# Performance work log

Measured on AMD Instinct MI355X. Metric: run time of the kernel, lower is better.

Reference implementation:

```python
import jax, jax.numpy as jnp
import numpy as np

N_HEADS = 12

def setup_inputs() -> dict:
    key = jax.random.key(0)
    ks = jax.random.split(key, 3)
    B, C, T = 4, 768, 2048
    x = jax.random.normal(ks[0], (B, C, T), dtype=jnp.float32)
    mask = jnp.ones((B, 1, 1, T), dtype=jnp.int32)  # all valid; masked_fill where mask==0
    Wqkv = jax.random.normal(ks[1], (3 * C, C), dtype=jnp.float32) * 0.02
    bqkv = jnp.zeros((3 * C,), dtype=jnp.float32)
    Wout = jax.random.normal(ks[2], (C, C), dtype=jnp.float32) * 0.02
    bout = jnp.zeros((C,), dtype=jnp.float32)
    return {"x": x, "mask": mask, "Wqkv": Wqkv, "bqkv": bqkv, "Wout": Wout, "bout": bout}


def reference(x, mask, Wqkv, bqkv, Wout, bout):
    B, C, T = x.shape
    H = N_HEADS
    d = C // H
    scale = 1.0 / jnp.sqrt(jnp.asarray(d, x.dtype))
    # 1x1 Conv1d == per-timestep matmul over channels
    qkv = jnp.einsum('oc,bct->bot', Wqkv, x) + bqkv[None, :, None]  # [B,3C,T]
    # channel dim splits as [3, H, d] per the torch view(B,3,H,d,T)
    qkv = qkv.reshape(B, 3, H, d, T).transpose(0, 1, 2, 4, 3)       # [B,3,H,T,d]
    q, k, v = qkv[:, 0], qkv[:, 1], qkv[:, 2]
    score = jnp.einsum('bhtd,bhsd->bhts', q, k) * scale             # [B,H,T,T]
    score = jnp.where(mask == 0, jnp.asarray(-10000.0, score.dtype), score)
    attn = jax.nn.softmax(score, axis=-1)  # dropout: eval mode (identity)
    o = jnp.einsum('bhts,bhsd->bhtd', attn, v)                      # [B,H,T,d]
    o = o.transpose(0, 1, 3, 2).reshape(B, C, T)                    # [B,C,T]
    return jnp.einsum('oc,bct->bot', Wout, o) + bout[None, :, None]
```

## Files before the change

kernel.cpp:

```cpp
#include <hip/hip_runtime.h>
#include <hip/hip_bf16.h>
#include <stdint.h>

#define B_   4
#define C_   768
#define T_   2048
#define H_   12
#define D_   64
#define O3_  2304

typedef __attribute__((ext_vector_type(4))) float f32x4;
typedef __attribute__((ext_vector_type(8))) short bf16x8;

__device__ __forceinline__ unsigned short f2bf(float f) {
  union { float f; unsigned int u; } v; v.f = f;
  unsigned int r = v.u + 0x7fffu + ((v.u >> 16) & 1u);
  return (unsigned short)(r >> 16);
}

__device__ __forceinline__ unsigned int pack2bf(float a, float b) {
  __hip_bfloat162 h2 = __float22bfloat162_rn(make_float2(a, b));
  union { __hip_bfloat162 h; unsigned int u; } cv; cv.h = h2;
  return cv.u;
}

__device__ __forceinline__ float fexp2(float x) {
#if __has_builtin(__builtin_amdgcn_exp2f)
  return __builtin_amdgcn_exp2f(x);
#else
  return exp2f(x);
#endif
}

__device__ __forceinline__ void async16(const void* g, void* lds) {
#if __has_builtin(__builtin_amdgcn_global_load_lds)
  __builtin_amdgcn_global_load_lds((const __attribute__((address_space(1))) void*)g,
                                   (__attribute__((address_space(3))) void*)lds, 16, 0, 0);
#else
  int lane = threadIdx.x & 63;
  *((uint4*)((char*)lds + lane * 16)) = *((const uint4*)g);
#endif
}


__global__ void cvt_f32_bf16(const float* __restrict__ in,
                             unsigned short* __restrict__ out, int n4) {
  int i = blockIdx.x * 256 + threadIdx.x;
  if (i < n4) {
    float4 f = ((const float4*)in)[i];
    ushort4 o;
    o.x = f2bf(f.x); o.y = f2bf(f.y); o.z = f2bf(f.z); o.w = f2bf(f.w);
    ((ushort4*)out)[i] = o;
  }
}

__global__ void make_bias(const int* __restrict__ mask, float* __restrict__ mbias, int n) {
  int i = blockIdx.x * 256 + threadIdx.x;
  if (i < n) mbias[i] = (mask[i] == 0) ? -14426.950408f : 0.0f;
}

__global__ void transpose_x(const float* __restrict__ x,
                            unsigned short* __restrict__ xT) {
  __shared__ unsigned short tile[32][33];
  int b = blockIdx.z;
  int c0 = blockIdx.y * 32;
  int t0 = blockIdx.x * 32;
  int tid = threadIdx.x;
  {
    int cl = tid >> 3;
    int tl = (tid & 7) * 4;
    float4 f = *(const float4*)(x + ((size_t)b * C_ + c0 + cl) * T_ + t0 + tl);
    tile[tl + 0][cl] = f2bf(f.x);
    tile[tl + 1][cl] = f2bf(f.y);
    tile[tl + 2][cl] = f2bf(f.z);
    tile[tl + 3][cl] = f2bf(f.w);
  }
  __syncthreads();
  {
    int tl = tid >> 3;
    int cl = (tid & 7) * 4;
    ushort4 o;
    o.x = tile[tl][cl + 0]; o.y = tile[tl][cl + 1];
    o.z = tile[tl][cl + 2]; o.w = tile[tl][cl + 3];
    *(ushort4*)(xT + ((size_t)b * T_ + t0 + tl) * C_ + c0 + cl) = o;
  }
}

__global__ __launch_bounds__(256)
void gemm_qkv(const unsigned short* __restrict__ xT,
              const unsigned short* __restrict__ W1,
              const float* __restrict__ bqkv,
              unsigned short* __restrict__ Qb,
              unsigned short* __restrict__ Kb,
              unsigned short* __restrict__ Vb) {
  __shared__ unsigned short sA[2][128 * 32];
  __shared__ unsigned short sB[2][128 * 32];

  const int b   = blockIdx.z;
  const int o0  = blockIdx.y * 128;
  const int t0  = blockIdx.x * 128;
  const int tid = threadIdx.x;
  const int wave = tid >> 6, lane = tid & 63;
  const int q = lane >> 4, ln = lane & 15;
  const int tw = wave >> 1, ow = wave & 1;

  const unsigned short* Ax = xT + (size_t)b * T_ * C_;
  const int srow = lane >> 2;
  const int scol = (lane & 3) * 8;

  const f32x4 ZERO = {0.f, 0.f, 0.f, 0.f};
  f32x4 acc[4][4];
#pragma unroll
  for (int mi = 0; mi < 4; ++mi)
#pragma unroll
    for (int ni = 0; ni < 4; ++ni) acc[mi][ni] = ZERO;

#pragma unroll
  for (int j = 0; j < 2; ++j) {
    const int chunk = wave * 2 + j;
    const int row = chunk * 16 + srow;
    async16(Ax + (size_t)(t0 + row) * C_ + scol, &sA[0][chunk * 512]);
    async16(W1 + (size_t)(o0 + row) * C_ + scol, &sB[0][chunk * 512]);
  }

  for (int i = 0; i < 24; ++i) {
    const int buf = i & 1;
    __syncthreads();
    if (i < 23) {
      const int k0 = (i + 1) * 32;
#pragma unroll
      for (int j = 0; j < 2; ++j) {
        const int chunk = wave * 2 + j;
        const int row = chunk * 16 + srow;
        async16(Ax + (size_t)(t0 + row) * C_ + k0 + scol, &sA[buf ^ 1][chunk * 512]);
        async16(W1 + (size_t)(o0 + row) * C_ + k0 + scol, &sB[buf ^ 1][chunk * 512]);
      }
    }

    bf16x8 aF[4], bF[4];
#pragma unroll
    for (int mi = 0; mi < 4; ++mi)
      aF[mi] = *(const bf16x8*)(&sA[buf][(tw * 64 + mi * 16 + ln) * 32 + q * 8]);
#pragma unroll
    for (int ni = 0; ni < 4; ++ni)
      bF[ni] = *(const bf16x8*)(&sB[buf][(ow * 64 + ni * 16 + ln) * 32 + q * 8]);
#pragma unroll
    for (int mi = 0; mi < 4; ++mi)
#pragma unroll
      for (int ni = 0; ni < 4; ++ni)
        acc[mi][ni] = __builtin_amdgcn_mfma_f32_16x16x32_bf16(aF[mi], bF[ni], acc[mi][ni], 0, 0, 0);
  }

  const float QSCL = 0.125f * 1.44269504f;
#pragma unroll
  for (int ni = 0; ni < 4; ++ni) {
    const int o = o0 + ow * 64 + ni * 16 + ln;
    const float bias = bqkv[o];
    const int which = o / C_;
    const int rem = o - which * C_;
    const int bh = b * H_ + (rem >> 6);
    const int dd = rem & 63;
#pragma unroll
    for (int mi = 0; mi < 4; ++mi) {
      const int tb = t0 + tw * 64 + mi * 16 + q * 4;
      f32x4 v = acc[mi][ni];
      if (which == 0) {
#pragma unroll
        for (int r = 0; r < 4; ++r)
          Qb[((size_t)bh * T_ + tb + r) * D_ + dd] = f2bf((v[r] + bias) * QSCL);
      } else if (which == 1) {
#pragma unroll
        for (int r = 0; r < 4; ++r) {
          const int s = tb + r;
          const int cp = (dd >> 3) ^ (s & 7);
          Kb[((size_t)bh * T_ + s) * 64 + (cp << 3) + (dd & 7)] = f2bf(v[r] + bias);
        }
      } else {
        const int tile = tb >> 6, si = tb & 63;
        const int cp = (si >> 3) ^ (dd & 7);
        ushort4 pk;
        pk.x = f2bf(v[0] + bias);
        pk.y = f2bf(v[1] + bias);
        pk.z = f2bf(v[2] + bias);
        pk.w = f2bf(v[3] + bias);
        *(ushort4*)(Vb + (((size_t)bh * 32 + tile) * 64 + dd) * 64 + (cp << 3) + (si & 7)) = pk;
      }
    }
  }
}

__global__ __launch_bounds__(256, 3)
void attn(const unsigned short* __restrict__ Qb,
          const unsigned short* __restrict__ Kb,
          const unsigned short* __restrict__ Vb,
          const float* __restrict__ mbias,
          unsigned short* __restrict__ Ob) {
  __shared__ __align__(16) char smem[53248];
  unsigned short* sK0 = (unsigned short*)smem;
  unsigned short* sV0 = (unsigned short*)(smem + 16384);

  const int id = blockIdx.x;
  const int bh = id % 48;
  const int tblk = id / 48;
  const int b = bh / H_, h = bh % H_;
  const int tid = threadIdx.x, wave = tid >> 6, lane = tid & 63;
  const int q = lane >> 4, ln = lane & 15;
  const int wj = wave & 1, si = wave >> 1;
  const int t0w = tblk * 128 + wj * 64;
  unsigned short* sPw = (unsigned short*)(smem + 32768 + wave * 5120);

  bf16x8 Qa[4][2];
#pragma unroll
  for (int tt = 0; tt < 4; ++tt) {
    const unsigned short* qrow = Qb + ((size_t)bh * T_ + t0w + tt * 16 + ln) * D_;
    Qa[tt][0] = *(const bf16x8*)(qrow + q * 8);
    Qa[tt][1] = *(const bf16x8*)(qrow + 32 + q * 8);
  }

  const f32x4 ZERO = {0.f, 0.f, 0.f, 0.f};
  f32x4 Oacc[4][4];
  f32x4 lacc[4];
#pragma unroll
  for (int dt = 0; dt < 4; ++dt)
#pragma unroll
    for (int tt = 0; tt < 4; ++tt) Oacc[dt][tt] = ZERO;
#pragma unroll
  for (int tt = 0; tt < 4; ++tt) lacc[tt] = ZERO;

  const short one_s = (ln == 0) ? (short)0x3F80 : (short)0;
  bf16x8 ones;
#pragma unroll
  for (int j = 0; j < 8; ++j) ones[j] = one_s;

  const unsigned short* gK = Kb + (size_t)bh * T_ * 64;
  const unsigned short* gV = Vb + (size_t)bh * 32 * 4096;

#pragma unroll
  for (int j = 0; j < 2; ++j) {
    const int chunk = wave * 2 + j;
    async16(gK + chunk * 512 + lane * 8, sK0 + chunk * 512);
    async16(gV + chunk * 512 + lane * 8, sV0 + chunk * 512);
  }

  for (int it = 0; it < 32; ++it) {
    const int buf = it & 1;
    __syncthreads();
    if (it < 31) {
      const unsigned short* k = gK + (it + 1) * 4096;
      const unsigned short* v = gV + (it + 1) * 4096;
      unsigned short* dK = sK0 + (buf ^ 1) * 4096;
      unsigned short* dV = sV0 + (buf ^ 1) * 4096;
#pragma unroll
      for (int j = 0; j < 2; ++j) {
        const int chunk = wave * 2 + j;
        async16(k + chunk * 512 + lane * 8, dK + chunk * 512);
        async16(v + chunk * 512 + lane * 8, dV + chunk * 512);
      }
    }

    const int s0 = it * 64;
    const float bvl = mbias[b * T_ + s0 + lane];
    const bool anymask = (__ballot(bvl != 0.0f) != 0ull);
    const unsigned short* sKc = sK0 + buf * 4096;
    const unsigned short* sVc = sV0 + buf * 4096;

#pragma unroll
    for (int sb = 0; sb < 2; ++sb) {
      const unsigned short* krow = sKc + (si * 32 + sb * 16 + ln) * 64;
      bf16x8 kf0 = *(const bf16x8*)(krow + ((q ^ (ln & 7)) << 3));
      bf16x8 kf1 = *(const bf16x8*)(krow + (((4 + q) ^ (ln & 7)) << 3));
      f32x4 bb = ZERO;
      if (anymask) bb = *(const f32x4*)(mbias + b * T_ + s0 + si * 32 + sb * 16 + q * 4);
#pragma unroll
      for (int tt = 0; tt < 4; ++tt) {
        f32x4 p0 = __builtin_amdgcn_mfma_f32_16x16x32_bf16(kf0, Qa[tt][0], ZERO, 0, 0, 0);
        f32x4 sc = __builtin_amdgcn_mfma_f32_16x16x32_bf16(kf1, Qa[tt][1], p0, 0, 0, 0);
        if (anymask) {
#pragma unroll
          for (int r = 0; r < 4; ++r) sc[r] += bb[r];
        }
        uint2 w;
        w.x = pack2bf(fexp2(sc[0]), fexp2(sc[1]));
        w.y = pack2bf(fexp2(sc[2]), fexp2(sc[3]));
        *(uint2*)(sPw + (tt * 16 + ln) * 40 + sb * 16 + q * 4) = w;
      }
    }

    bf16x8 vf[4];
#pragma unroll
    for (int dt = 0; dt < 4; ++dt)
      vf[dt] = *(const bf16x8*)(sVc + (dt * 16 + ln) * 64 +
                                (((si * 4 + q) ^ (ln & 7)) << 3));
#pragma unroll
    for (int tt = 0; tt < 4; ++tt) {
      bf16x8 pf = *(const bf16x8*)(sPw + (tt * 16 + ln) * 40 + q * 8);
      lacc[tt] = __builtin_amdgcn_mfma_f32_16x16x32_bf16(ones, pf, lacc[tt], 0, 0, 0);
#pragma unroll
      for (int dt = 0; dt < 4; ++dt)
        Oacc[dt][tt] = __builtin_amdgcn_mfma_f32_16x16x32_bf16(vf[dt], pf, Oacc[dt][tt], 0, 0, 0);
    }
  }

  __syncthreads();
  float* fbuf = (float*)smem;
  float* lbuf = (float*)(smem + 34816);
  if (si == 1) {
#pragma unroll
    for (int tt = 0; tt < 4; ++tt) {
#pragma unroll
      for (int dt = 0; dt < 4; ++dt)
        *(f32x4*)(fbuf + ((size_t)(wj * 64 + tt * 16 + ln)) * 68 + dt * 16 + q * 4) = Oacc[dt][tt];
      if (q == 0) lbuf[wj * 64 + tt * 16 + ln] = lacc[tt][0];
    }
  }
  __syncthreads();
  if (si == 0) {
#pragma unroll
    for (int tt = 0; tt < 4; ++tt) {
      const float lv = __shfl(lacc[tt][0], ln, 64) + lbuf[wj * 64 + tt * 16 + ln];
      const float inv = 1.0f / lv;
      const int t = t0w + tt * 16 + ln;
#pragma unroll
      for (int dt = 0; dt < 4; ++dt) {
        f32x4 o = Oacc[dt][tt];
        f32x4 p = *(const f32x4*)(fbuf + ((size_t)(wj * 64 + tt * 16 + ln)) * 68 + dt * 16 + q * 4);
        ushort4 pk;
        pk.x = f2bf((o[0] + p[0]) * inv);
        pk.y = f2bf((o[1] + p[1]) * inv);
        pk.z = f2bf((o[2] + p[2]) * inv);
        pk.w = f2bf((o[3] + p[3]) * inv);
        *(ushort4*)(Ob + ((size_t)b * T_ + t) * C_ + h * D_ + dt * 16 + q * 4) = pk;
      }
    }
  }
}

__global__ __launch_bounds__(256)
void gemm_out(const unsigned short* __restrict__ Ob,
              const unsigned short* __restrict__ W2,
              const float* __restrict__ bout,
              float* __restrict__ out) {
  __shared__ unsigned short sA[2][128 * 32];
  __shared__ unsigned short sB[2][128 * 32];

  const int b   = blockIdx.z;
  const int o0  = blockIdx.y * 128;
  const int t0  = blockIdx.x * 128;
  const int tid = threadIdx.x;
  const int wave = tid >> 6, lane = tid & 63;
  const int q = lane >> 4, ln = lane & 15;
  const int tw = wave >> 1, ow = wave & 1;

  const unsigned short* Bo = Ob + (size_t)b * T_ * C_;
  const int srow = lane >> 2;
  const int scol = (lane & 3) * 8;

  const f32x4 ZERO = {0.f, 0.f, 0.f, 0.f};
  f32x4 acc[4][4];
#pragma unroll
  for (int mi = 0; mi < 4; ++mi)
#pragma unroll
    for (int ni = 0; ni < 4; ++ni) acc[mi][ni] = ZERO;

#pragma unroll
  for (int j = 0; j < 2; ++j) {
    const int chunk = wave * 2 + j;
    const int row = chunk * 16 + srow;
    async16(W2 + (size_t)(o0 + row) * C_ + scol, &sA[0][chunk * 512]);
    async16(Bo + (size_t)(t0 + row) * C_ + scol, &sB[0][chunk * 512]);
  }

  for (int i = 0; i < 24; ++i) {
    const int buf = i & 1;
    __syncthreads();
    if (i < 23) {
      const int k0 = (i + 1) * 32;
#pragma unroll
      for (int j = 0; j < 2; ++j) {
        const int chunk = wave * 2 + j;
        const int row = chunk * 16 + srow;
        async16(W2 + (size_t)(o0 + row) * C_ + k0 + scol, &sA[buf ^ 1][chunk * 512]);
        async16(Bo + (size_t)(t0 + row) * C_ + k0 + scol, &sB[buf ^ 1][chunk * 512]);
      }
    }

    bf16x8 aF[4], bF[4];
#pragma unroll
    for (int mi = 0; mi < 4; ++mi)
      aF[mi] = *(const bf16x8*)(&sA[buf][(tw * 64 + mi * 16 + ln) * 32 + q * 8]);
#pragma unroll
    for (int ni = 0; ni < 4; ++ni)
      bF[ni] = *(const bf16x8*)(&sB[buf][(ow * 64 + ni * 16 + ln) * 32 + q * 8]);
#pragma unroll
    for (int mi = 0; mi < 4; ++mi)
#pragma unroll
      for (int ni = 0; ni < 4; ++ni)
        acc[mi][ni] = __builtin_amdgcn_mfma_f32_16x16x32_bf16(aF[mi], bF[ni], acc[mi][ni], 0, 0, 0);
  }

#pragma unroll
  for (int mi = 0; mi < 4; ++mi) {
    const int ob = o0 + tw * 64 + mi * 16 + q * 4;
#pragma unroll
    for (int ni = 0; ni < 4; ++ni) {
      const int t = t0 + ow * 64 + ni * 16 + ln;
      f32x4 v = acc[mi][ni];
#pragma unroll
      for (int r = 0; r < 4; ++r)
        out[((size_t)b * C_ + ob + r) * T_ + t] = v[r] + bout[ob + r];
    }
  }
}


extern "C" void kernel_launch(void* const* d_in, const int* in_sizes, int n_in,
                              void* d_out, int out_size, void* d_ws, size_t ws_size,
                              hipStream_t stream) {
  (void)in_sizes; (void)n_in; (void)out_size; (void)ws_size;
  const float* x    = (const float*)d_in[0];
  const int*   mask = (const int*)d_in[1];
  const float* Wqkv = (const float*)d_in[2];
  const float* bqkv = (const float*)d_in[3];
  const float* Wout = (const float*)d_in[4];
  const float* bout = (const float*)d_in[5];
  float* out = (float*)d_out;

  const size_t szHead = (size_t)B_ * H_ * T_ * D_;
  const size_t szBTC  = (size_t)B_ * T_ * C_;
  unsigned short* Qb  = (unsigned short*)d_ws;
  unsigned short* Kb  = Qb + szHead;
  unsigned short* Vb  = Kb + szHead;
  unsigned short* Ob  = Vb + szHead;
  unsigned short* xT  = Ob + szBTC;
  unsigned short* W1b = xT + szBTC;
  unsigned short* W2b = W1b + (size_t)O3_ * C_;
  float* mbias        = (float*)(W2b + (size_t)C_ * C_);

  cvt_f32_bf16<<<dim3((O3_ * C_ / 4 + 255) / 256), 256, 0, stream>>>(Wqkv, W1b, O3_ * C_ / 4);
  cvt_f32_bf16<<<dim3((C_ * C_ / 4 + 255) / 256), 256, 0, stream>>>(Wout, W2b, C_ * C_ / 4);
  make_bias<<<dim3((B_ * T_ + 255) / 256), 256, 0, stream>>>(mask, mbias, B_ * T_);
  transpose_x<<<dim3(T_ / 32, C_ / 32, B_), 256, 0, stream>>>(x, xT);
  gemm_qkv<<<dim3(T_ / 128, O3_ / 128, B_), 256, 0, stream>>>(xT, W1b, bqkv, Qb, Kb, Vb);
  attn<<<dim3(768), 256, 0, stream>>>(Qb, Kb, Vb, mbias, Ob);
  gemm_out<<<dim3(T_ / 128, C_ / 128, B_), 256, 0, stream>>>(Ob, W2b, bout, out);
}
```

Baseline: 238.0 us.

## Keep softmax probabilities in registers via fp16 MFMA and split keys across four waves

The attention kernel now gives each block 64 queries and splits every 64-key tile across four waves of 16 keys each. Exponentiated scores are packed into fp16 registers and fed straight to 16x16x16 f16 MFMAs, with V stored in fp16, so the LDS round-trip for P and the ones-vector MFMA for the row sum are gone. The row sum is accumulated in scalar registers and reduced with shuffles. The grid doubles, LDS drops so more blocks fit per CU, and the partial outputs of the four waves are reduced through fp16 LDS buffers, which costs extra cross-wave reduction and precision.

New measurement: 327.5 us. 37.6% more time.

```diff
diff --git a/kernel.cpp b/kernel.cpp
--- a/kernel.cpp
+++ b/kernel.cpp
@@ -11,6 +11,8 @@
 
 typedef __attribute__((ext_vector_type(4))) float f32x4;
 typedef __attribute__((ext_vector_type(8))) short bf16x8;
+typedef __attribute__((ext_vector_type(4))) _Float16 f16x4;
+typedef __attribute__((ext_vector_type(2))) __fp16 h16x2;
 
 __device__ __forceinline__ unsigned short f2bf(float f) {
   union { float f; unsigned int u; } v; v.f = f;
@@ -18,10 +20,12 @@
   return (unsigned short)(r >> 16);
 }
 
-__device__ __forceinline__ unsigned int pack2bf(float a, float b) {
-  __hip_bfloat162 h2 = __float22bfloat162_rn(make_float2(a, b));
-  union { __hip_bfloat162 h; unsigned int u; } cv; cv.h = h2;
-  return cv.u;
+__device__ __forceinline__ unsigned short f2h(float f) {
+  union { _Float16 h; unsigned short u; } c; c.h = (_Float16)f; return c.u;
+}
+
+__device__ __forceinline__ float h2f(unsigned short u) {
+  union { _Float16 h; unsigned short u; } c; c.u = u; return (float)c.h;
 }
 
 __device__ __forceinline__ float fexp2(float x) {
@@ -179,23 +183,23 @@
         const int tile = tb >> 6, si = tb & 63;
         const int cp = (si >> 3) ^ (dd & 7);
         ushort4 pk;
-        pk.x = f2bf(v[0] + bias);
-        pk.y = f2bf(v[1] + bias);
-        pk.z = f2bf(v[2] + bias);
-        pk.w = f2bf(v[3] + bias);
+        pk.x = f2h(v[0] + bias);
+        pk.y = f2h(v[1] + bias);
+        pk.z = f2h(v[2] + bias);
+        pk.w = f2h(v[3] + bias);
         *(ushort4*)(Vb + (((size_t)bh * 32 + tile) * 64 + dd) * 64 + (cp << 3) + (si & 7)) = pk;
       }
     }
   }
 }
 
-__global__ __launch_bounds__(256, 3)
+__global__ __launch_bounds__(256, 4)
 void attn(const unsigned short* __restrict__ Qb,
           const unsigned short* __restrict__ Kb,
           const unsigned short* __restrict__ Vb,
           const float* __restrict__ mbias,
           unsigned short* __restrict__ Ob) {
-  __shared__ __align__(16) char smem[53248];
+  __shared__ __align__(16) char smem[32768];
   unsigned short* sK0 = (unsigned short*)smem;
   unsigned short* sV0 = (unsigned short*)(smem + 16384);
 
@@ -203,41 +207,32 @@
   const int bh = id % 48;
   const int tblk = id / 48;
   const int b = bh / H_, h = bh % H_;
-  const int tid = threadIdx.x, wave = tid >> 6, lane = tid & 63;
+  const int tid = threadIdx.x, si = tid >> 6, lane = tid & 63;
   const int q = lane >> 4, ln = lane & 15;
-  const int wj = wave & 1, si = wave >> 1;
-  const int t0w = tblk * 128 + wj * 64;
-  unsigned short* sPw = (unsigned short*)(smem + 32768 + wave * 5120);
+  const int t0 = tblk * 64;
 
   bf16x8 Qa[4][2];
 #pragma unroll
   for (int tt = 0; tt < 4; ++tt) {
-    const unsigned short* qrow = Qb + ((size_t)bh * T_ + t0w + tt * 16 + ln) * D_;
+    const unsigned short* qrow = Qb + ((size_t)bh * T_ + t0 + tt * 16 + ln) * D_;
     Qa[tt][0] = *(const bf16x8*)(qrow + q * 8);
     Qa[tt][1] = *(const bf16x8*)(qrow + 32 + q * 8);
   }
 
   const f32x4 ZERO = {0.f, 0.f, 0.f, 0.f};
   f32x4 Oacc[4][4];
-  f32x4 lacc[4];
-#pragma unroll
-  for (int dt = 0; dt < 4; ++dt)
-#pragma unroll
-    for (int tt = 0; tt < 4; ++tt) Oacc[dt][tt] = ZERO;
-#pragma unroll
-  for (int tt = 0; tt < 4; ++tt) lacc[tt] = ZERO;
-
-  const short one_s = (ln == 0) ? (short)0x3F80 : (short)0;
-  bf16x8 ones;
-#pragma unroll
-  for (int j = 0; j < 8; ++j) ones[j] = one_s;
+  float lac[4] = {0.f, 0.f, 0.f, 0.f};
+#pragma unroll
+  for (int tt = 0; tt < 4; ++tt)
+#pragma unroll
+    for (int dt = 0; dt < 4; ++dt) Oacc[tt][dt] = ZERO;
 
   const unsigned short* gK = Kb + (size_t)bh * T_ * 64;
   const unsigned short* gV = Vb + (size_t)bh * 32 * 4096;
 
 #pragma unroll
   for (int j = 0; j < 2; ++j) {
-    const int chunk = wave * 2 + j;
+    const int chunk = si * 2 + j;
     async16(gK + chunk * 512 + lane * 8, sK0 + chunk * 512);
     async16(gV + chunk * 512 + lane * 8, sV0 + chunk * 512);
   }
@@ -252,7 +247,7 @@
       unsigned short* dV = sV0 + (buf ^ 1) * 4096;
 #pragma unroll
       for (int j = 0; j < 2; ++j) {
-        const int chunk = wave * 2 + j;
+        const int chunk = si * 2 + j;
         async16(k + chunk * 512 + lane * 8, dK + chunk * 512);
         async16(v + chunk * 512 + lane * 8, dV + chunk * 512);
       }
@@ -264,72 +259,86 @@
     const unsigned short* sKc = sK0 + buf * 4096;
     const unsigned short* sVc = sV0 + buf * 4096;
 
-#pragma unroll
-    for (int sb = 0; sb < 2; ++sb) {
-      const unsigned short* krow = sKc + (si * 32 + sb * 16 + ln) * 64;
-      bf16x8 kf0 = *(const bf16x8*)(krow + ((q ^ (ln & 7)) << 3));
-      bf16x8 kf1 = *(const bf16x8*)(krow + (((4 + q) ^ (ln & 7)) << 3));
-      f32x4 bb = ZERO;
-      if (anymask) bb = *(const f32x4*)(mbias + b * T_ + s0 + si * 32 + sb * 16 + q * 4);
-#pragma unroll
-      for (int tt = 0; tt < 4; ++tt) {
-        f32x4 p0 = __builtin_amdgcn_mfma_f32_16x16x32_bf16(kf0, Qa[tt][0], ZERO, 0, 0, 0);
-        f32x4 sc = __builtin_amdgcn_mfma_f32_16x16x32_bf16(kf1, Qa[tt][1], p0, 0, 0, 0);
-        if (anymask) {
-#pragma unroll
-          for (int r = 0; r < 4; ++r) sc[r] += bb[r];
-        }
-        uint2 w;
-        w.x = pack2bf(fexp2(sc[0]), fexp2(sc[1]));
-        w.y = pack2bf(fexp2(sc[2]), fexp2(sc[3]));
-        *(uint2*)(sPw + (tt * 16 + ln) * 40 + sb * 16 + q * 4) = w;
-      }
-    }
-
-    bf16x8 vf[4];
-#pragma unroll
-    for (int dt = 0; dt < 4; ++dt)
-      vf[dt] = *(const bf16x8*)(sVc + (dt * 16 + ln) * 64 +
-                                (((si * 4 + q) ^ (ln & 7)) << 3));
+    const unsigned short* krow = sKc + (si * 16 + ln) * 64;
+    bf16x8 kf0 = *(const bf16x8*)(krow + ((q ^ (ln & 7)) << 3));
+    bf16x8 kf1 = *(const bf16x8*)(krow + (((4 + q) ^ (ln & 7)) << 3));
+
+    f32x4 bb = ZERO;
+    if (anymask) bb = *(const f32x4*)(mbias + b * T_ + s0 + si * 16 + q * 4);
+
+    f16x4 Pf[4];
 #pragma unroll
     for (int tt = 0; tt < 4; ++tt) {
-      bf16x8 pf = *(const bf16x8*)(sPw + (tt * 16 + ln) * 40 + q * 8);
-      lacc[tt] = __builtin_amdgcn_mfma_f32_16x16x32_bf16(ones, pf, lacc[tt], 0, 0, 0);
+      f32x4 p0 = __builtin_amdgcn_mfma_f32_16x16x32_bf16(kf0, Qa[tt][0], ZERO, 0, 0, 0);
+      f32x4 sc = __builtin_amdgcn_mfma_f32_16x16x32_bf16(kf1, Qa[tt][1], p0, 0, 0, 0);
+      if (anymask) {
+#pragma unroll
+        for (int r = 0; r < 4; ++r) sc[r] += bb[r];
+      }
+      float e0 = fexp2(sc[0]), e1 = fexp2(sc[1]);
+      float e2 = fexp2(sc[2]), e3 = fexp2(sc[3]);
+      lac[tt] += (e0 + e1) + (e2 + e3);
+      union { h16x2 h2[2]; f16x4 h4; } u;
+      u.h2[0] = __builtin_amdgcn_cvt_pkrtz(e0, e1);
+      u.h2[1] = __builtin_amdgcn_cvt_pkrtz(e2, e3);
+      Pf[tt] = u.h4;
+    }
+
+#pragma unroll
+    for (int dt = 0; dt < 4; ++dt) {
+      f16x4 vf = *(const f16x4*)(sVc + (dt * 16 + ln) * 64 +
+                                 (((si * 2 + (q >> 1)) ^ (ln & 7)) << 3) + ((q & 1) << 2));
+#pragma unroll
+      for (int tt = 0; tt < 4; ++tt)
+        Oacc[tt][dt] = __builtin_amdgcn_mfma_f32_16x16x16f16(Pf[tt], vf, Oacc[tt][dt], 0, 0, 0);
+    }
+  }
+
+#pragma unroll
+  for (int tt = 0; tt < 4; ++tt) {
+    lac[tt] += __shfl_xor(lac[tt], 16, 64);
+    lac[tt] += __shfl_xor(lac[tt], 32, 64);
+  }
+
+  __syncthreads();
+  unsigned short* hbuf = (unsigned short*)smem;
+  float* lbuf = (float*)(smem + 24576);
+  if (si > 0) {
+    const int base = (si - 1) * 4096;
+#pragma unroll
+    for (int tt = 0; tt < 4; ++tt) {
 #pragma unroll
       for (int dt = 0; dt < 4; ++dt)
-        Oacc[dt][tt] = __builtin_amdgcn_mfma_f32_16x16x32_bf16(vf[dt], pf, Oacc[dt][tt], 0, 0, 0);
-    }
-  }
-
-  __syncthreads();
-  float* fbuf = (float*)smem;
-  float* lbuf = (float*)(smem + 34816);
-  if (si == 1) {
-#pragma unroll
-    for (int tt = 0; tt < 4; ++tt) {
-#pragma unroll
-      for (int dt = 0; dt < 4; ++dt)
-        *(f32x4*)(fbuf + ((size_t)(wj * 64 + tt * 16 + ln)) * 68 + dt * 16 + q * 4) = Oacc[dt][tt];
-      if (q == 0) lbuf[wj * 64 + tt * 16 + ln] = lacc[tt][0];
+#pragma unroll
+        for (int r = 0; r < 4; ++r)
+          hbuf[base + (tt * 16 + q * 4 + r) * 64 + dt * 16 + ln] = f2h(Oacc[tt][dt][r]);
+      if (q == 0) lbuf[(si - 1) * 64 + tt * 16 + ln] = lac[tt];
     }
   }
   __syncthreads();
   if (si == 0) {
 #pragma unroll
     for (int tt = 0; tt < 4; ++tt) {
-      const float lv = __shfl(lacc[tt][0], ln, 64) + lbuf[wj * 64 + tt * 16 + ln];
-      const float inv = 1.0f / lv;
-      const int t = t0w + tt * 16 + ln;
+      float inv[4];
+#pragma unroll
+      for (int r = 0; r < 4; ++r) {
+        const int tl = tt * 16 + q * 4 + r;
+        float l = __shfl(lac[tt], q * 4 + r, 64);
+        l += lbuf[tl] + lbuf[64 + tl] + lbuf[128 + tl];
+        inv[r] = 1.0f / l;
+      }
 #pragma unroll
       for (int dt = 0; dt < 4; ++dt) {
-        f32x4 o = Oacc[dt][tt];
-        f32x4 p = *(const f32x4*)(fbuf + ((size_t)(wj * 64 + tt * 16 + ln)) * 68 + dt * 16 + q * 4);
-        ushort4 pk;
-        pk.x = f2bf((o[0] + p[0]) * inv);
-        pk.y = f2bf((o[1] + p[1]) * inv);
-        pk.z = f2bf((o[2] + p[2]) * inv);
-        pk.w = f2bf((o[3] + p[3]) * inv);
-        *(ushort4*)(Ob + ((size_t)b * T_ + t) * C_ + h * D_ + dt * 16 + q * 4) = pk;
+#pragma unroll
+        for (int r = 0; r < 4; ++r) {
+          const int tl = tt * 16 + q * 4 + r;
+          const int dl = dt * 16 + ln;
+          float o = Oacc[tt][dt][r]
+                  + h2f(hbuf[tl * 64 + dl])
+                  + h2f(hbuf[4096 + tl * 64 + dl])
+                  + h2f(hbuf[8192 + tl * 64 + dl]);
+          Ob[((size_t)b * T_ + t0 + tl) * C_ + h * D_ + dl] = f2bf(o * inv[r]);
+        }
       }
     }
   }
@@ -441,6 +450,6 @@
   make_bias<<<dim3((B_ * T_ + 255) / 256), 256, 0, stream>>>(mask, mbias, B_ * T_);
   transpose_x<<<dim3(T_ / 32, C_ / 32, B_), 256, 0, stream>>>(x, xT);
   gemm_qkv<<<dim3(T_ / 128, O3_ / 128, B_), 256, 0, stream>>>(xT, W1b, bqkv, Qb, Kb, Vb);
-  attn<<<dim3(768), 256, 0, stream>>>(Qb, Kb, Vb, mbias, Ob);
+  attn<<<dim3(1536), 256, 0, stream>>>(Qb, Kb, Vb, mbias, Ob);
   gemm_out<<<dim3(T_ / 128, C_ / 128, B_), 256, 0, stream>>>(Ob, W2b, bout, out);
 }
```
